# Kernel tuning notes

Hardware: AMD Instinct MI355X
Metric: run time of the kernel (lower is better)

The kernel has to match this reference:

```python
import jax, jax.numpy as jnp
import numpy as np

H, W, C, UP = 32, 32, 1024, 2  # num_patch=(32,32), embed_dim=1024, upsample_rate=2


def setup_inputs() -> dict:
    key = jax.random.key(0)
    k1, k2 = jax.random.split(key)
    x = jax.random.normal(k1, (32, H * W, C), dtype=jnp.float32)
    # keras Conv2D 1x1 kernel (1,1,Cin,Cout) squeezed to (Cin, Cout); Cin = Cout = C//UP
    w = jax.random.normal(k2, (C // UP, C // UP), dtype=jnp.float32) * 0.02
    return {"x": x, "w": w}


def reference(x, w):
    B, L, Cin = x.shape
    assert L == H * W and Cin == C
    xg = x.reshape(B, H, W, C)
    x0 = xg[..., : C // UP]        # [B,H,W,C/2]
    x1 = xg[..., C // UP:]         # [B,H,W,C/2]
    # Row-wise interleave: output rows alternate x0[i], x1[i] -> [B, 2H, W, C/2]
    xi = jnp.stack([x0, x1], axis=2).reshape(B, 2 * H, W, C // UP)
    # 1x1 conv (no bias) == per-pixel linear projection C/2 -> C/2
    y = jnp.einsum('bhwc,cd->bhwd', xi, w)
    # return_vector=True: tokens [B, 2L, C//2]
    return y.reshape(B, L * UP, C // 2)
```

## Files before the change

### kernel.cpp

```cpp
#include <hip/hip_runtime.h>
#include <hip/hip_bf16.h>
#include <stdint.h>

typedef __attribute__((ext_vector_type(4))) float f32x4;
typedef __attribute__((ext_vector_type(16))) float f32x16;
typedef __attribute__((ext_vector_type(8))) short bf16x8;
typedef __attribute__((ext_vector_type(4))) uint32_t u32x4;

#define KD 512
#define ND 512

__device__ __forceinline__ uint32_t pk_bf16(float lo, float hi) {
  uint32_t ulo = __float_as_uint(lo) + 0x8000u;
  uint32_t uhi = __float_as_uint(hi) + 0x8000u;
  return __builtin_amdgcn_perm(uhi, ulo, 0x07060302u);
}

__global__ void wt_kernel(const float* __restrict__ w, uint16_t* __restrict__ wt) {
  __shared__ float tile[32][33];
  const int bx = blockIdx.x, by = blockIdx.y;
  const int tx = threadIdx.x, ty = threadIdx.y;
#pragma unroll
  for (int i = 0; i < 32; i += 8)
    tile[ty + i][tx] = w[(bx * 32 + ty + i) * ND + by * 32 + tx];
  __syncthreads();
#pragma unroll
  for (int i = 0; i < 32; i += 8) {
    uint32_t u = __float_as_uint(tile[tx][ty + i]);
    uint32_t r = (u + 0x7FFFu + ((u >> 16) & 1u)) >> 16;
    const int d = by * 32 + ty + i;
    const int k = bx * 32 + tx;
    wt[((k >> 4) * 512 + d) * 16 + ((k >> 3) & 1) * 8 + (k & 7)] = (uint16_t)r;
  }
}

__global__ __launch_bounds__(512, 4) void gemm_kernel(
    const float* __restrict__ x, const uint16_t* __restrict__ wt,
    float* __restrict__ out) {
  __shared__ uint16_t As[64 * 512];

  const int tid = threadIdx.x;
  const int lane = tid & 63;
  const int l31 = lane & 31, hi = lane >> 5;
  const int wid = tid >> 6;
  const int m0 = blockIdx.x * 64;

  {
    const int r = tid >> 3;
    const int c0 = tid & 7;
    const int aRow = m0 + ((r & 31) << 1) + (r >> 5);
    const char* src = (const char*)x + (size_t)aRow * (KD * 4) + c0 * 32;
    char* dst = (char*)As + r * 1024;
    const int rx = (r & 7) << 1;
#pragma unroll
    for (int i = 0; i < 8; ++i) {
      const int c = c0 + i * 8;
      f32x4 lo = *(const f32x4*)(src + i * 256);
      f32x4 h4 = *(const f32x4*)(src + i * 256 + 16);
      u32x4 p = {pk_bf16(lo.x, lo.y), pk_bf16(lo.z, lo.w),
                 pk_bf16(h4.x, h4.y), pk_bf16(h4.z, h4.w)};
      *(u32x4*)(dst + (c ^ rx) * 16) = p;
    }
  }
  __syncthreads();

  const char* wb = (const char*)wt;
  uint32_t wOff[2];
#pragma unroll
  for (int tn = 0; tn < 2; ++tn)
    wOff[tn] = (uint32_t)(wid * 64 + tn * 32 + l31) * 32 + hi * 16;

  const uint32_t ax = (l31 & 7) << 1;
  uint32_t aBase[2];
#pragma unroll
  for (int rg = 0; rg < 2; ++rg) aBase[rg] = (rg * 32 + l31) * 1024;

  f32x16 acc[2][2];
#pragma unroll
  for (int rg = 0; rg < 2; ++rg)
#pragma unroll
    for (int tn = 0; tn < 2; ++tn)
#pragma unroll
      for (int e = 0; e < 16; ++e) acc[rg][tn][e] = 0.f;

  bf16x8 wf[4][2];
#pragma unroll
  for (int ks = 0; ks < 3; ++ks)
#pragma unroll
    for (int tn = 0; tn < 2; ++tn)
      wf[ks][tn] = *(const bf16x8*)(wb + ks * 16384 + wOff[tn]);

#pragma unroll
  for (int ks = 0; ks < 32; ++ks) {
    if (ks + 3 < 32) {
#pragma unroll
      for (int tn = 0; tn < 2; ++tn)
        wf[(ks + 3) & 3][tn] =
            *(const bf16x8*)(wb + (ks + 3) * 16384 + wOff[tn]);
    }
    bf16x8 af[2];
#pragma unroll
    for (int rg = 0; rg < 2; ++rg) {
      const uint32_t s = (uint32_t)(2 * ks + hi) ^ ax;
      af[rg] = *(const bf16x8*)((const char*)As + aBase[rg] + s * 16);
    }
#pragma unroll
    for (int rg = 0; rg < 2; ++rg)
#pragma unroll
      for (int tn = 0; tn < 2; ++tn)
        acc[rg][tn] = __builtin_amdgcn_mfma_f32_32x32x16_bf16(
            wf[ks & 3][tn], af[rg], acc[rg][tn], 0, 0, 0);
  }

#pragma unroll
  for (int rg = 0; rg < 2; ++rg) {
    float* op = out + (size_t)(m0 + rg * 32 + l31) * ND + wid * 64;
#pragma unroll
    for (int tn = 0; tn < 2; ++tn) {
#pragma unroll
      for (int q = 0; q < 4; ++q) {
        f32x4 v = {acc[rg][tn][q * 4 + 0], acc[rg][tn][q * 4 + 1],
                   acc[rg][tn][q * 4 + 2], acc[rg][tn][q * 4 + 3]};
        *(f32x4*)(op + tn * 32 + q * 8 + hi * 4) = v;
      }
    }
  }
}

extern "C" void kernel_launch(void* const* d_in, const int* in_sizes, int n_in,
                              void* d_out, int out_size, void* d_ws, size_t ws_size,
                              hipStream_t stream) {
  const float* x = (const float*)d_in[0];
  const float* w = (const float*)d_in[1];
  float* out = (float*)d_out;
  uint16_t* wt = (uint16_t*)d_ws;

  wt_kernel<<<dim3(16, 16), dim3(32, 8), 0, stream>>>(w, wt);
  gemm_kernel<<<dim3(1024), dim3(512), 0, stream>>>(x, wt, out);
}
```

Measured before the change: 254.8 us.

## Double-buffer A tiles in K-chunks and process two M-tiles per block

Replaces the single full-K A load (64x512 bf16 in LDS) with a double-buffered pipeline over 128-wide K chunks. The global loads for the next chunk are issued before the MFMAs on the current one, and the bf16 convert and LDS store happen after them. Each block now handles two 64-row M tiles (512 blocks instead of 1024), and the loop carries over between tiles. LDS use drops, which may allow more blocks per CU, but the new schedule adds a barrier for every chunk.

Result: slower. 260.2 us (+2.1%).

```diff
diff --git a/kernel.cpp b/kernel.cpp
--- a/kernel.cpp
+++ b/kernel.cpp
@@ -37,43 +37,31 @@
 __global__ __launch_bounds__(512, 4) void gemm_kernel(
     const float* __restrict__ x, const uint16_t* __restrict__ wt,
     float* __restrict__ out) {
-  __shared__ uint16_t As[64 * 512];
+  __shared__ uint16_t As[2][64 * 128];
 
   const int tid = threadIdx.x;
   const int lane = tid & 63;
   const int l31 = lane & 31, hi = lane >> 5;
   const int wid = tid >> 6;
-  const int m0 = blockIdx.x * 64;
+  const int mblk = blockIdx.x * 128;
 
-  {
-    const int r = tid >> 3;
-    const int c0 = tid & 7;
-    const int aRow = m0 + ((r & 31) << 1) + (r >> 5);
-    const char* src = (const char*)x + (size_t)aRow * (KD * 4) + c0 * 32;
-    char* dst = (char*)As + r * 1024;
-    const int rx = (r & 7) << 1;
-#pragma unroll
-    for (int i = 0; i < 8; ++i) {
-      const int c = c0 + i * 8;
-      f32x4 lo = *(const f32x4*)(src + i * 256);
-      f32x4 h4 = *(const f32x4*)(src + i * 256 + 16);
-      u32x4 p = {pk_bf16(lo.x, lo.y), pk_bf16(lo.z, lo.w),
-                 pk_bf16(h4.x, h4.y), pk_bf16(h4.z, h4.w)};
-      *(u32x4*)(dst + (c ^ rx) * 16) = p;
-    }
-  }
-  __syncthreads();
+  const int sr = tid >> 3;
+  const int sc = tid & 7;
+  const int prow = ((sr & 31) << 1) + (sr >> 5);
+  const char* xrow = (const char*)x + (size_t)(mblk + prow) * 2048 + sc * 32;
+  const int srx = (sr & 7) << 1;
+  const int dOff0 = sr * 256 + ((sc) ^ srx) * 16;
+  const int dOff1 = sr * 256 + ((sc + 8) ^ srx) * 16;
 
   const char* wb = (const char*)wt;
   uint32_t wOff[2];
 #pragma unroll
   for (int tn = 0; tn < 2; ++tn)
     wOff[tn] = (uint32_t)(wid * 64 + tn * 32 + l31) * 32 + hi * 16;
-
+  uint32_t aOff[2];
+#pragma unroll
+  for (int rg = 0; rg < 2; ++rg) aOff[rg] = (uint32_t)(rg * 32 + l31) * 256;
   const uint32_t ax = (l31 & 7) << 1;
-  uint32_t aBase[2];
-#pragma unroll
-  for (int rg = 0; rg < 2; ++rg) aBase[rg] = (rg * 32 + l31) * 1024;
 
   f32x16 acc[2][2];
 #pragma unroll
@@ -83,45 +71,91 @@
 #pragma unroll
       for (int e = 0; e < 16; ++e) acc[rg][tn][e] = 0.f;
 
-  bf16x8 wf[4][2];
-#pragma unroll
-  for (int ks = 0; ks < 3; ++ks)
-#pragma unroll
-    for (int tn = 0; tn < 2; ++tn)
-      wf[ks][tn] = *(const bf16x8*)(wb + ks * 16384 + wOff[tn]);
+  f32x4 sv0, sv1, sv2, sv3;
+
+  auto ISSUE = [&](int it) {
+    const char* s = xrow + (it >> 2) * (64 * 2048) + (it & 3) * 512;
+    sv0 = *(const f32x4*)(s);
+    sv1 = *(const f32x4*)(s + 16);
+    sv2 = *(const f32x4*)(s + 256);
+    sv3 = *(const f32x4*)(s + 256 + 16);
+  };
+  auto COMMIT = [&](int it) {
+    char* d = (char*)As[it & 1];
+    u32x4 p0 = {pk_bf16(sv0.x, sv0.y), pk_bf16(sv0.z, sv0.w),
+                pk_bf16(sv1.x, sv1.y), pk_bf16(sv1.z, sv1.w)};
+    u32x4 p1 = {pk_bf16(sv2.x, sv2.y), pk_bf16(sv2.z, sv2.w),
+                pk_bf16(sv3.x, sv3.y), pk_bf16(sv3.z, sv3.w)};
+    *(u32x4*)(d + dOff0) = p0;
+    *(u32x4*)(d + dOff1) = p1;
+  };
+
+  ISSUE(0);
+  COMMIT(0);
 
 #pragma unroll
-  for (int ks = 0; ks < 32; ++ks) {
-    if (ks + 3 < 32) {
+  for (int it = 0; it < 8; ++it) {
+    __syncthreads();
+    if (it < 7) ISSUE(it + 1);
+
+    {
+      const char* ab = (const char*)As[it & 1];
+      const int gks0 = (it & 3) * 8;
+      bf16x8 wf[4][2];
 #pragma unroll
-      for (int tn = 0; tn < 2; ++tn)
-        wf[(ks + 3) & 3][tn] =
-            *(const bf16x8*)(wb + (ks + 3) * 16384 + wOff[tn]);
+      for (int kp = 0; kp < 3; ++kp)
+#pragma unroll
+        for (int tn = 0; tn < 2; ++tn)
+          wf[kp][tn] =
+              *(const bf16x8*)(wb + (size_t)(gks0 + kp) * 16384 + wOff[tn]);
+#pragma unroll
+      for (int ksl = 0; ksl < 8; ++ksl) {
+        if (ksl < 5) {
+#pragma unroll
+          for (int tn = 0; tn < 2; ++tn)
+            wf[(ksl + 3) & 3][tn] = *(const bf16x8*)(
+                wb + (size_t)(gks0 + ksl + 3) * 16384 + wOff[tn]);
+        }
+        bf16x8 af[2];
+#pragma unroll
+        for (int rg = 0; rg < 2; ++rg) {
+          const uint32_t s = ((uint32_t)(2 * ksl + hi)) ^ ax;
+          af[rg] = *(const bf16x8*)(ab + aOff[rg] + s * 16);
+        }
+#pragma unroll
+        for (int rg = 0; rg < 2; ++rg)
+#pragma unroll
+          for (int tn = 0; tn < 2; ++tn)
+            acc[rg][tn] = __builtin_amdgcn_mfma_f32_32x32x16_bf16(
+                wf[ksl & 3][tn], af[rg], acc[rg][tn], 0, 0, 0);
+      }
     }
-    bf16x8 af[2];
+
+    if (it < 7) COMMIT(it + 1);
+
+    if ((it & 3) == 3) {
+      const int p = it >> 2;
 #pragma unroll
-    for (int rg = 0; rg < 2; ++rg) {
-      const uint32_t s = (uint32_t)(2 * ks + hi) ^ ax;
-      af[rg] = *(const bf16x8*)((const char*)As + aBase[rg] + s * 16);
-    }
+      for (int rg = 0; rg < 2; ++rg) {
+        float* op =
+            out + (size_t)(mblk + p * 64 + rg * 32 + l31) * ND + wid * 64;
 #pragma unroll
-    for (int rg = 0; rg < 2; ++rg)
+        for (int tn = 0; tn < 2; ++tn) {
 #pragma unroll
-      for (int tn = 0; tn < 2; ++tn)
-        acc[rg][tn] = __builtin_amdgcn_mfma_f32_32x32x16_bf16(
-            wf[ks & 3][tn], af[rg], acc[rg][tn], 0, 0, 0);
-  }
-
+          for (int q = 0; q < 4; ++q) {
+            f32x4 v = {acc[rg][tn][q * 4 + 0], acc[rg][tn][q * 4 + 1],
+                       acc[rg][tn][q * 4 + 2], acc[rg][tn][q * 4 + 3]};
+            *(f32x4*)(op + tn * 32 + q * 8 + hi * 4) = v;
+          }
+        }
+      }
+      if (it == 3) {
 #pragma unroll
-  for (int rg = 0; rg < 2; ++rg) {
-    float* op = out + (size_t)(m0 + rg * 32 + l31) * ND + wid * 64;
+        for (int rg = 0; rg < 2; ++rg)
 #pragma unroll
-    for (int tn = 0; tn < 2; ++tn) {
+          for (int tn = 0; tn < 2; ++tn)
 #pragma unroll
-      for (int q = 0; q < 4; ++q) {
-        f32x4 v = {acc[rg][tn][q * 4 + 0], acc[rg][tn][q * 4 + 1],
-                   acc[rg][tn][q * 4 + 2], acc[rg][tn][q * 4 + 3]};
-        *(f32x4*)(op + tn * 32 + q * 8 + hi * 4) = v;
+            for (int e = 0; e < 16; ++e) acc[rg][tn][e] = 0.f;
       }
     }
   }
@@ -136,5 +170,5 @@
   uint16_t* wt = (uint16_t*)d_ws;
 
   wt_kernel<<<dim3(16, 16), dim3(32, 8), 0, stream>>>(w, wt);
-  gemm_kernel<<<dim3(1024), dim3(512), 0, stream>>>(x, wt, out);
+  gemm_kernel<<<dim3(512), dim3(512), 0, stream>>>(x, wt, out);
 }
```
